# Kernel tuning notes

Measured on AMD Instinct MI355X. Metric: run time of the kernel, lower is better.

Reference implementation:

```python
import jax, jax.numpy as jnp
import numpy as np

B, H, W = 16, 512, 1024
MAXK = 512            # cfg.MAX_KEYPOINTS
R = 3                 # cfg.NMS_RADIUS
K = 2 * R + 1         # max-pool kernel size
N = 4 * MAXK          # candidate pool size (max_keypoints * 4)


def setup_inputs() -> dict:
    key = jax.random.key(0)
    k1, k2 = jax.random.split(key)
    gray_image = jax.random.uniform(k1, (B, 1, H, W), dtype=jnp.float32)
    mask = jax.random.uniform(k2, (B, 1, H, W), dtype=jnp.float32)
    return {"gray_image": gray_image, "mask": mask}


def _detect_one(img, m):
    # img, m: [H, W]
    # local-max via max-pool (torch max_pool2d implicitly pads with -inf)
    pooled = jax.lax.reduce_window(img, -jnp.inf, jax.lax.max,
                                   (K, K), (1, 1), [(R, R), (R, R)])
    valid = (img == pooled) & (img > 0.1) & (m > 0)

    flat_img = img.reshape(-1)
    flat_scores = jnp.where(valid.reshape(-1), flat_img, -jnp.inf)
    # fixed-size candidate pool: top 4*MAXK scores (descending, matches torch.topk)
    top_sc, top_idx = jax.lax.top_k(flat_scores, N)
    cand_valid = jnp.isfinite(top_sc)                 # slots beyond #valid points

    xs = (top_idx % W).astype(jnp.float32)
    ys = (top_idx // W).astype(jnp.float32)
    kp = jnp.stack([xs, ys], axis=1)                  # [N, 2] (x, y) order
    sc = jnp.where(cand_valid, flat_img[top_idx], 0.0)  # [N], differentiable gather

    # pairwise euclidean distances (torch.cdist)
    diff = kp[:, None, :] - kp[None, :, :]            # [N, N, 2]
    dist = jnp.sqrt(jnp.sum(diff * diff, axis=-1))    # [N, N]

    # greedy sequential NMS in score order (candidates already sorted descending)
    ar = jnp.arange(N)

    def body(i, keep):
        suppress = (dist[i] < R) & (ar != i)
        return jnp.where(keep[i], keep & ~suppress, keep)

    keep = jax.lax.fori_loop(0, N, body, cand_valid)
    keep = jax.lax.stop_gradient(keep)

    # compact kept points (score order) into fixed [MAXK] output, zero-padded
    pos = jnp.cumsum(keep.astype(jnp.int32)) - 1
    slot = jnp.where(keep & (pos < MAXK), pos, MAXK)  # MAXK = dump slot
    kp_out = jnp.zeros((MAXK + 1, 2), kp.dtype).at[slot].set(kp)[:MAXK]
    sc_out = jnp.zeros((MAXK + 1,), sc.dtype).at[slot].set(sc)[:MAXK]
    return kp_out, sc_out


def reference(gray_image, mask):
    img = (gray_image * mask)[:, 0]   # [B, H, W]
    m = mask[:, 0]
    return jax.vmap(_detect_one)(img, m)  # ([B, MAXK, 2], [B, MAXK])
```

## Files before the change

### kernel.cpp

```cpp
#include <hip/hip_runtime.h>
#include <cstdint>
#include <cstddef>

#define Bn 16
#define Hn 512
#define Wn 1024
#define NTOP 2048
#define KMAX 512
#define PAIRCAP 2048
#define FBINS 4096
#define FBASE 126566
#define KEYSN 4096
#define XS 18
#define XW 58
#define SLOTS_B 256
#define BLKS (XS * 4)
#define NSLOT (BLKS * SLOTS_B)

__global__ __launch_bounds__(256) void detect_kernel(const float* __restrict__ gray,
                                                     const float* __restrict__ mask,
                                                     uint64_t* __restrict__ slots) {
    __shared__ uint64_t s_list[SLOTS_B];
    __shared__ int s_n;

    const int s    = blockIdx.x;
    const int yB   = blockIdx.y;
    const int b    = blockIdx.z;
    const int t    = threadIdx.x;
    const int lane = t & 63;
    const int w    = t >> 6;
    const int col  = s * XW - 3 + lane;
    const int ybase = yB * 128 + w * 32;

    if (t == 0) s_n = 0;
    __syncthreads();

    const float* gb = gray + (size_t)b * Hn * Wn;
    const float* mb = mask + (size_t)b * Hn * Wn;
    const int colc = col < 0 ? 0 : (col >= Wn ? Wn - 1 : col);
    const bool colok = (col >= 0) && (col < Wn);
    const float NINF = -__builtin_inff();

    float im[38];
#pragma unroll
    for (int rr = 0; rr < 38; ++rr) {
        int gy = ybase - 3 + rr;
        int gyc = gy < 0 ? 0 : (gy >= Hn ? Hn - 1 : gy);
        size_t o = (size_t)gyc * Wn + colc;
        float val = gb[o] * mb[o];
        im[rr] = (colok && gy >= 0 && gy < Hn) ? val : NINF;
    }

#pragma unroll
    for (int r = 0; r < 32; ++r) {
        float v7 = fmaxf(fmaxf(fmaxf(im[r], im[r + 1]), fmaxf(im[r + 2], im[r + 3])),
                         fmaxf(fmaxf(im[r + 4], im[r + 5]), im[r + 6]));
        float s1 = fmaxf(v7, __shfl_down(v7, 1, 64));
        float s2 = fmaxf(s1, __shfl_down(s1, 2, 64));
        float s3 = fmaxf(s2, __shfl_down(s2, 3, 64));
        float h  = __shfl_up(s3, 3, 64);
        float v  = im[r + 3];
        if (lane >= 3 && lane <= 60 && col < Wn && v == h && v > 0.1f) {
            uint32_t idx = (uint32_t)((ybase + r) * Wn + col);
            uint64_t key = ((uint64_t)__float_as_uint(v) << 32) | (uint32_t)(~idx);
            int pos = atomicAdd(&s_n, 1);
            if (pos < SLOTS_B) s_list[pos] = key;
        }
    }
    __syncthreads();

    int m = s_n; if (m > SLOTS_B) m = SLOTS_B;
    const int blk = yB * XS + s;
    uint64_t* dst = slots + ((size_t)b * BLKS + blk) * SLOTS_B;
    dst[t] = (t < m) ? s_list[t] : 0ull;
}

__global__ __launch_bounds__(1024) void topk_nms_kernel(const uint64_t* __restrict__ slots,
                                                        float* __restrict__ kp_out,
                                                        float* __restrict__ sc_out) {
    __shared__ uint64_t keys[KEYSN];
    __shared__ uint64_t keys2[NTOP];
    __shared__ int      hist[FBINS];
    __shared__ int      sfx[FBINS];
    __shared__ int      scanA[64];
    __shared__ uint32_t pairs[PAIRCAP];
    __shared__ uint8_t  keep[NTOP];
    __shared__ int      sel[KMAX];
    __shared__ int      misc[4];

    const int b = blockIdx.x;
    const int t = threadIdx.x;
    const int lane = t & 63;
    const int w = t >> 6;
    const ulonglong2* sb2 = (const ulonglong2*)(slots + (size_t)b * NSLOT);

    *(int4*)&hist[t << 2] = make_int4(0, 0, 0, 0);
    for (int i = t; i < NTOP; i += 1024) keys2[i] = 0ull;
    if (t < 4) misc[t] = 0;
    if (t < KMAX) sel[t] = -1;
    __syncthreads();

    for (int i = t; i < NSLOT / 2; i += 1024) {
        ulonglong2 kp = sb2[i];
#pragma unroll
        for (int h = 0; h < 2; ++h) {
            uint32_t sbits = (uint32_t)((h ? kp.y : kp.x) >> 32);
            if (sbits) {
                int bin = (int)(sbits >> 13) - FBASE;
                bin = bin < 0 ? 0 : (bin > FBINS - 1 ? FBINS - 1 : bin);
                atomicAdd(&hist[bin], 1);
            }
        }
    }
    __syncthreads();

    const int base4 = t << 2;
    const int4 h4 = *(const int4*)&hist[base4];
    int loc = h4.x + h4.y + h4.z + h4.w;
    int x = loc;
#pragma unroll
    for (int d = 1; d < 64; d <<= 1) {
        int y = __shfl_down(x, d, 64);
        if (lane + d < 64) x += y;
    }
    if (lane == 0) scanA[w] = x;
    __syncthreads();
    if (w == 0) {
        int v = (lane < 16) ? scanA[lane] : 0;
#pragma unroll
        for (int d = 1; d < 16; d <<= 1) {
            int y = __shfl_down(v, d, 64);
            if (lane + d < 64) v += y;
        }
        if (lane < 16) scanA[lane] = v;
    }
    __syncthreads();
    const int total = scanA[0];
    const int target = total < NTOP ? total : NTOP;
    const int S_incl = x + ((w < 15) ? scanA[w + 1] : 0);

    int r = S_incl - loc;
    int s3 = r + h4.w;
    int s2 = s3 + h4.z;
    int s1 = s2 + h4.y;
    int s0 = s1 + h4.x;
    *(int4*)&sfx[base4]  = make_int4(s0, s1, s2, s3);
    *(int4*)&hist[base4] = make_int4(s1, s2, s3, r);
    if (s0 >= target && s1 < target) misc[2] = base4;
    if (s1 >= target && s2 < target) misc[2] = base4 + 1;
    if (s2 >= target && s3 < target) misc[2] = base4 + 2;
    if (s3 >= target && (base4 + 3 == FBINS - 1 || r < target)) misc[2] = base4 + 3;
    __syncthreads();
    const int T = misc[2];
    int cnt = sfx[T]; if (cnt > KEYSN) cnt = KEYSN;

    for (int i = t; i < NSLOT / 2; i += 1024) {
        ulonglong2 kp = sb2[i];
#pragma unroll
        for (int h = 0; h < 2; ++h) {
            uint64_t key = h ? kp.y : kp.x;
            uint32_t sbits = (uint32_t)(key >> 32);
            if (sbits) {
                int bin = (int)(sbits >> 13) - FBASE;
                bin = bin < 0 ? 0 : (bin > FBINS - 1 ? FBINS - 1 : bin);
                if (bin >= T) {
                    int pos = atomicAdd(&hist[bin], 1);
                    if (pos < KEYSN) keys[pos] = key;
                }
            }
        }
    }
    __syncthreads();

    for (int e = t; e < cnt; e += 1024) {
        uint64_t key = keys[e];
        uint32_t sbits = (uint32_t)(key >> 32);
        int bin = (int)(sbits >> 13) - FBASE;
        bin = bin < 0 ? 0 : (bin > FBINS - 1 ? FBINS - 1 : bin);
        int a0 = (bin + 1 < FBINS) ? sfx[bin + 1] : 0;
        int e0 = sfx[bin]; if (e0 > KEYSN) e0 = KEYSN;
        int rank = a0;
        for (int q = a0; q < e0; ++q) rank += (keys[q] > key) ? 1 : 0;
        if (rank < NTOP) keys2[rank] = key;
    }
    __syncthreads();

    for (int j = t; j < NTOP; j += 1024) {
        uint32_t s = (uint32_t)(keys2[j] >> 32);
        keep[j] = (s != 0u) ? 1 : 0;
        if (s) {
            uint32_t idx = ~(uint32_t)keys2[j];
            int xq = (int)(idx & (Wn - 1)), yq = (int)(idx >> 10);
            for (int i = j - 1; i >= 0 && (uint32_t)(keys2[i] >> 32) == s; --i) {
                uint32_t idx2 = ~(uint32_t)keys2[i];
                int dx = xq - (int)(idx2 & (Wn - 1));
                int dy = yq - (int)(idx2 >> 10);
                if (dx * dx + dy * dy < 9) {
                    int p = atomicAdd(&misc[1], 1);
                    if (p < PAIRCAP) pairs[p] = ((uint32_t)j << 16) | (uint32_t)i;
                }
            }
        }
    }
    __syncthreads();

    if (t == 0) {
        int pc = misc[1]; if (pc > PAIRCAP) pc = PAIRCAP;
        for (int a = 1; a < pc; ++a) {
            uint32_t v = pairs[a]; int q = a - 1;
            while (q >= 0 && pairs[q] > v) { pairs[q + 1] = pairs[q]; --q; }
            pairs[q + 1] = v;
        }
        for (int a = 0; a < pc; ++a) {
            int j = (int)(pairs[a] >> 16), i = (int)(pairs[a] & 0xFFFF);
            if (keep[i]) keep[j] = 0;
        }
    }
    __syncthreads();

    int j0 = 2 * t, j1 = j0 + 1;
    int k0 = keep[j0], k1 = keep[j1];
    int sum = k0 + k1;
    int xp = sum;
#pragma unroll
    for (int d = 1; d < 64; d <<= 1) {
        int y = __shfl_up(xp, d, 64);
        if (lane >= d) xp += y;
    }
    if (lane == 63) scanA[w] = xp;
    __syncthreads();
    if (w == 0) {
        int v = (lane < 16) ? scanA[lane] : 0;
#pragma unroll
        for (int d = 1; d < 16; d <<= 1) {
            int y = __shfl_up(v, d, 64);
            if (lane >= d) v += y;
        }
        if (lane < 16) scanA[lane] = v;
    }
    __syncthreads();
    int pre = xp + ((w > 0) ? scanA[w - 1] : 0);
    int ex = pre - sum;
    if (k0 && ex < KMAX) sel[ex] = j0;
    if (k1 && (ex + k0) < KMAX) sel[ex + k0] = j1;
    __syncthreads();

    if (t < KMAX) {
        int jj = sel[t];
        float xo = 0.f, yo = 0.f, so = 0.f;
        if (jj >= 0) {
            uint32_t idx = ~(uint32_t)keys2[jj];
            xo = (float)(idx & (Wn - 1));
            yo = (float)(idx >> 10);
            so = __uint_as_float((uint32_t)(keys2[jj] >> 32));
        }
        kp_out[(size_t)b * KMAX * 2 + 2 * t]     = xo;
        kp_out[(size_t)b * KMAX * 2 + 2 * t + 1] = yo;
        sc_out[(size_t)b * KMAX + t]             = so;
    }
}

extern "C" void kernel_launch(void* const* d_in, const int* in_sizes, int n_in,
                              void* d_out, int out_size, void* d_ws, size_t ws_size,
                              hipStream_t stream) {
    const float* gray = (const float*)d_in[0];
    const float* mask = (const float*)d_in[1];
    float* out = (float*)d_out;
    float* kp_out = out;
    float* sc_out = out + (size_t)Bn * KMAX * 2;

    uint64_t* slots = (uint64_t*)d_ws;

    dim3 g1(XS, 4, Bn);
    detect_kernel<<<g1, 256, 0, stream>>>(gray, mask, slots);
    topk_nms_kernel<<<Bn, 1024, 0, stream>>>(slots, kp_out, sc_out);
}
```

Baseline: 45.03 us.

## Process two columns per lane with float2 loads and cache slot keys in registers

The detect kernel now has each lane load two adjacent columns via float2, which halves the number of column strips (each strip is wider with more slots per block). The horizontal 7-wide max is rebuilt from per-lane pair maxima using a few cross-lane shuffles. The top-k kernel loads its per-image slot keys once into registers (9 ulonglong2 per thread) and reuses them for both the histogram and scatter passes instead of reading global memory twice. This cuts global load instructions and halo overhead, at the cost of more registers and a fixed unroll that assumes NSLOT/2 equals 9*1024.

```diff
diff --git a/kernel.cpp b/kernel.cpp
--- a/kernel.cpp
+++ b/kernel.cpp
@@ -11,9 +11,9 @@
 #define FBINS 4096
 #define FBASE 126566
 #define KEYSN 4096
-#define XS 18
-#define XW 58
-#define SLOTS_B 256
+#define XS 9
+#define XW 122
+#define SLOTS_B 512
 #define BLKS (XS * 4)
 #define NSLOT (BLKS * SLOTS_B)
 
@@ -29,7 +29,8 @@
     const int t    = threadIdx.x;
     const int lane = t & 63;
     const int w    = t >> 6;
-    const int col  = s * XW - 3 + lane;
+    const int xb   = s * XW - 4;
+    const int c0   = xb + 2 * lane;
     const int ybase = yB * 128 + w * 32;
 
     if (t == 0) s_n = 0;
@@ -37,32 +38,46 @@
 
     const float* gb = gray + (size_t)b * Hn * Wn;
     const float* mb = mask + (size_t)b * Hn * Wn;
-    const int colc = col < 0 ? 0 : (col >= Wn ? Wn - 1 : col);
-    const bool colok = (col >= 0) && (col < Wn);
+    const bool ok0 = (c0 >= 0) && (c0 < Wn);
+    const bool ok1 = (c0 + 1 >= 0) && (c0 + 1 < Wn);
+    const int cl = c0 < 0 ? 0 : (c0 > Wn - 2 ? Wn - 2 : c0);
     const float NINF = -__builtin_inff();
 
-    float im[38];
+    float2 im[38];
 #pragma unroll
     for (int rr = 0; rr < 38; ++rr) {
         int gy = ybase - 3 + rr;
         int gyc = gy < 0 ? 0 : (gy >= Hn ? Hn - 1 : gy);
-        size_t o = (size_t)gyc * Wn + colc;
-        float val = gb[o] * mb[o];
-        im[rr] = (colok && gy >= 0 && gy < Hn) ? val : NINF;
+        const float2 g = *(const float2*)(gb + (size_t)gyc * Wn + cl);
+        const float2 m = *(const float2*)(mb + (size_t)gyc * Wn + cl);
+        bool rok = (gy >= 0) && (gy < Hn);
+        im[rr].x = (rok && ok0) ? g.x * m.x : NINF;
+        im[rr].y = (rok && ok1) ? g.y * m.y : NINF;
     }
 
 #pragma unroll
     for (int r = 0; r < 32; ++r) {
-        float v7 = fmaxf(fmaxf(fmaxf(im[r], im[r + 1]), fmaxf(im[r + 2], im[r + 3])),
-                         fmaxf(fmaxf(im[r + 4], im[r + 5]), im[r + 6]));
-        float s1 = fmaxf(v7, __shfl_down(v7, 1, 64));
-        float s2 = fmaxf(s1, __shfl_down(s1, 2, 64));
-        float s3 = fmaxf(s2, __shfl_down(s2, 3, 64));
-        float h  = __shfl_up(s3, 3, 64);
-        float v  = im[r + 3];
-        if (lane >= 3 && lane <= 60 && col < Wn && v == h && v > 0.1f) {
-            uint32_t idx = (uint32_t)((ybase + r) * Wn + col);
-            uint64_t key = ((uint64_t)__float_as_uint(v) << 32) | (uint32_t)(~idx);
+        float ex = fmaxf(fmaxf(fmaxf(im[r].x, im[r+1].x), fmaxf(im[r+2].x, im[r+3].x)),
+                         fmaxf(fmaxf(im[r+4].x, im[r+5].x), im[r+6].x));
+        float ey = fmaxf(fmaxf(fmaxf(im[r].y, im[r+1].y), fmaxf(im[r+2].y, im[r+3].y)),
+                         fmaxf(fmaxf(im[r+4].y, im[r+5].y), im[r+6].y));
+        float p  = fmaxf(ex, ey);
+        float eyu2 = __shfl_up(ey, 2, 64);
+        float pu1  = __shfl_up(p, 1, 64);
+        float pd1  = __shfl_down(p, 1, 64);
+        float exd2 = __shfl_down(ex, 2, 64);
+        float win0 = fmaxf(fmaxf(eyu2, pu1), fmaxf(p, pd1));
+        float win1 = fmaxf(fmaxf(pu1, p), fmaxf(pd1, exd2));
+        float v0 = im[r + 3].x, v1 = im[r + 3].y;
+        if (lane >= 2 && lane <= 62 && ok0 && v0 == win0 && v0 > 0.1f) {
+            uint32_t idx = (uint32_t)((ybase + r) * Wn + c0);
+            uint64_t key = ((uint64_t)__float_as_uint(v0) << 32) | (uint32_t)(~idx);
+            int pos = atomicAdd(&s_n, 1);
+            if (pos < SLOTS_B) s_list[pos] = key;
+        }
+        if (lane >= 1 && lane <= 61 && ok1 && v1 == win1 && v1 > 0.1f) {
+            uint32_t idx = (uint32_t)((ybase + r) * Wn + c0 + 1);
+            uint64_t key = ((uint64_t)__float_as_uint(v1) << 32) | (uint32_t)(~idx);
             int pos = atomicAdd(&s_n, 1);
             if (pos < SLOTS_B) s_list[pos] = key;
         }
@@ -72,7 +87,11 @@
     int m = s_n; if (m > SLOTS_B) m = SLOTS_B;
     const int blk = yB * XS + s;
     uint64_t* dst = slots + ((size_t)b * BLKS + blk) * SLOTS_B;
-    dst[t] = (t < m) ? s_list[t] : 0ull;
+#pragma unroll
+    for (int k = 0; k < SLOTS_B / 256; ++k) {
+        int i = t + k * 256;
+        dst[i] = (i < m) ? s_list[i] : 0ull;
+    }
 }
 
 __global__ __launch_bounds__(1024) void topk_nms_kernel(const uint64_t* __restrict__ slots,
@@ -94,17 +113,21 @@
     const int w = t >> 6;
     const ulonglong2* sb2 = (const ulonglong2*)(slots + (size_t)b * NSLOT);
 
+    ulonglong2 ck[9];
+#pragma unroll
+    for (int k = 0; k < 9; ++k) ck[k] = sb2[t + (k << 10)];
+
     *(int4*)&hist[t << 2] = make_int4(0, 0, 0, 0);
     for (int i = t; i < NTOP; i += 1024) keys2[i] = 0ull;
     if (t < 4) misc[t] = 0;
     if (t < KMAX) sel[t] = -1;
     __syncthreads();
 
-    for (int i = t; i < NSLOT / 2; i += 1024) {
-        ulonglong2 kp = sb2[i];
+#pragma unroll
+    for (int k = 0; k < 9; ++k) {
 #pragma unroll
         for (int h = 0; h < 2; ++h) {
-            uint32_t sbits = (uint32_t)((h ? kp.y : kp.x) >> 32);
+            uint32_t sbits = (uint32_t)((h ? ck[k].y : ck[k].x) >> 32);
             if (sbits) {
                 int bin = (int)(sbits >> 13) - FBASE;
                 bin = bin < 0 ? 0 : (bin > FBINS - 1 ? FBINS - 1 : bin);
@@ -154,11 +177,11 @@
     const int T = misc[2];
     int cnt = sfx[T]; if (cnt > KEYSN) cnt = KEYSN;
 
-    for (int i = t; i < NSLOT / 2; i += 1024) {
-        ulonglong2 kp = sb2[i];
+#pragma unroll
+    for (int k = 0; k < 9; ++k) {
 #pragma unroll
         for (int h = 0; h < 2; ++h) {
-            uint64_t key = h ? kp.y : kp.x;
+            uint64_t key = h ? ck[k].y : ck[k].x;
             uint32_t sbits = (uint32_t)(key >> 32);
             if (sbits) {
                 int bin = (int)(sbits >> 13) - FBASE;
```

New measurement: 46.89 us. 4.1% more time.
